# Optimization experiments

Measured on AMD Instinct MI355X. Metric: run time of the kernel, lower is better.

## Reference

```python
import jax, jax.numpy as jnp
import numpy as np

N_NODES = 100000
N_EDGES = 600000
DIM_IN = 128
DIM_H = 128
DIM_OUT = 64
N_LAYERS = 3
BN_EPS = 1e-5


def setup_inputs() -> dict:
    key = jax.random.key(0)
    ks = jax.random.split(key, 10)
    x = jax.random.normal(ks[0], (N_NODES, DIM_IN), dtype=jnp.float32)
    edge_index = jax.random.randint(ks[1], (2, N_EDGES), 0, N_NODES, dtype=jnp.int64)
    s = 0.05
    conv_w1 = jax.random.normal(ks[2], (N_LAYERS, DIM_H, DIM_H), dtype=jnp.float32) * s
    conv_b1 = jnp.zeros((N_LAYERS, DIM_H), jnp.float32)
    conv_w2 = jax.random.normal(ks[3], (N_LAYERS, DIM_H, DIM_H), dtype=jnp.float32) * s
    conv_b2 = jnp.zeros((N_LAYERS, DIM_H), jnp.float32)
    bn_gamma = jnp.ones((N_LAYERS, DIM_H), jnp.float32)
    bn_beta = jnp.zeros((N_LAYERS, DIM_H), jnp.float32)
    fc1_w = jax.random.normal(ks[4], (DIM_H, DIM_H), dtype=jnp.float32) * s
    fc1_b = jnp.zeros((DIM_H,), jnp.float32)
    fc2_w = jax.random.normal(ks[5], (DIM_H, DIM_OUT), dtype=jnp.float32) * s
    fc2_b = jnp.zeros((DIM_OUT,), jnp.float32)
    # deterministic dropout mask, p=0.5, inverted-dropout scaling baked in (0 or 2)
    dropout_mask = (jax.random.uniform(ks[6], (N_NODES, DIM_H)) < 0.5).astype(jnp.float32) * 2.0
    return {"x": x, "edge_index": edge_index,
            "conv_w1": conv_w1, "conv_b1": conv_b1, "conv_w2": conv_w2, "conv_b2": conv_b2,
            "bn_gamma": bn_gamma, "bn_beta": bn_beta,
            "fc1_w": fc1_w, "fc1_b": fc1_b, "fc2_w": fc2_w, "fc2_b": fc2_b,
            "dropout_mask": dropout_mask}


def reference(x, edge_index, conv_w1, conv_b1, conv_w2, conv_b2,
              bn_gamma, bn_beta, fc1_w, fc1_b, fc2_w, fc2_b, dropout_mask):
    src, dst = edge_index[0], edge_index[1]
    n = x.shape[0]
    h = x
    for l in range(N_LAYERS):
        # GINConv (eps=0): (1+eps)*h + sum_{j->i} h_j, then 2-layer MLP
        agg = h + jax.ops.segment_sum(h[src], dst, num_segments=n)
        z = jnp.maximum(agg @ conv_w1[l] + conv_b1[l], 0.0) @ conv_w2[l] + conv_b2[l]
        z = jnp.maximum(z, 0.0)  # outer ReLU
        # BatchNorm1d (training mode: batch stats, biased variance)
        mean = z.mean(axis=0)
        var = z.var(axis=0)
        h = (z - mean) * jax.lax.rsqrt(var + BN_EPS) * bn_gamma[l] + bn_beta[l]
    h = jnp.maximum(h @ fc1_w + fc1_b, 0.0)
    h = h * dropout_mask  # dropout p=0.5 with precomputed inverted mask
    logits = h @ fc2_w + fc2_b
    return jax.nn.log_softmax(logits, axis=-1)
```

## Files before the change

### kernel.cpp

```cpp
#include <hip/hip_runtime.h>
#include <stdint.h>

#define N_NODES 100000
#define N_EDGES 600000
#define DIM_H   128
#define DIM_OUT 64
#define WPAD    136
#define BN_EPS  1e-5f
#define NBLK    391
#define GRID64_HEAD 1563
#define MLP_GRID 782

typedef __attribute__((ext_vector_type(8))) __bf16        bh8;
typedef __attribute__((ext_vector_type(4))) float         fl4;
typedef __attribute__((ext_vector_type(8))) unsigned short us8;
typedef __attribute__((ext_vector_type(4))) unsigned short us4;

__device__ __forceinline__ unsigned short f2bfbits(float f) {
  unsigned int u = __builtin_bit_cast(unsigned int, f);
  u += 0x7fffu + ((u >> 16) & 1u);
  return (unsigned short)(u >> 16);
}
__device__ __forceinline__ float bf2f(unsigned short b) {
  unsigned int u = ((unsigned int)b) << 16;
  return __builtin_bit_cast(float, u);
}
__device__ __forceinline__ void wave_lds_fence() {
  asm volatile("s_waitcnt lgkmcnt(0)" ::: "memory");
  __builtin_amdgcn_sched_barrier(0);
}

__global__ void prep_kernel(const float* __restrict__ cw1, const float* __restrict__ cw2,
                            const float* __restrict__ fc1w, const float* __restrict__ fc2w,
                            unsigned short* __restrict__ W1F, unsigned short* __restrict__ W2F,
                            unsigned short* __restrict__ F1F, unsigned short* __restrict__ F2F,
                            float* __restrict__ stats, int* __restrict__ deg,
                            unsigned short* __restrict__ zrow) {
  int t = blockIdx.x * 256 + threadIdx.x;
  if (t < 3 * 16384) {
    int l = t >> 14, o = t & 16383;
    int j = o & 7, lane = (o >> 3) & 63, kk = (o >> 9) & 3, n0 = o >> 11;
    int k = kk * 32 + ((lane >> 4) << 3) + j;
    int n = (n0 << 4) + (lane & 15);
    W1F[t] = f2bfbits(cw1[l * 16384 + k * 128 + n]);
    W2F[t] = f2bfbits(cw2[l * 16384 + k * 128 + n]);
  }
  if (t < 16384) {
    int o = t;
    int j = o & 7, lane = (o >> 3) & 63, kk = (o >> 9) & 3, n0 = o >> 11;
    int k = kk * 32 + ((lane >> 4) << 3) + j;
    int n = (n0 << 4) + (lane & 15);
    F1F[t] = f2bfbits(fc1w[k * 128 + n]);
  }
  if (t < 8192) {
    int o = t;
    int j = o & 7, lane = (o >> 3) & 63, kk = (o >> 9) & 3, n0 = o >> 11;
    int k = kk * 32 + ((lane >> 4) << 3) + j;
    int n = (n0 << 4) + (lane & 15);
    F2F[t] = f2bfbits(fc2w[k * 64 + n]);
  }
  if (t < 768)   stats[t] = 0.f;
  if (t < 128)   zrow[t] = 0;
  if (t < N_NODES) deg[t] = 0;
}

__global__ void deg_xcast(const float* __restrict__ x, unsigned short* __restrict__ xB,
                          const int* __restrict__ ei, int* __restrict__ deg,
                          const float* __restrict__ mask, unsigned int* __restrict__ bmask) {
  int i = blockIdx.x * 256 + threadIdx.x;
  fl4 v = reinterpret_cast<const fl4*>(x)[i];
  us4 p;
#pragma unroll
  for (int j = 0; j < 4; ++j) p[j] = f2bfbits(v[j]);
  reinterpret_cast<us4*>(xB)[i] = p;
  if (i < N_EDGES) atomicAdd(&deg[ei[N_EDGES + i]], 1);
  if (i < N_NODES * 4) {
    const float* mp = mask + (long)i * 32;
    unsigned int b = 0;
#pragma unroll
    for (int j8 = 0; j8 < 8; ++j8) {
      fl4 mv = *reinterpret_cast<const fl4*>(mp + j8 * 4);
      b |= (mv[0] > 0.f ? 1u : 0u) << (j8 * 4 + 0);
      b |= (mv[1] > 0.f ? 1u : 0u) << (j8 * 4 + 1);
      b |= (mv[2] > 0.f ? 1u : 0u) << (j8 * 4 + 2);
      b |= (mv[3] > 0.f ? 1u : 0u) << (j8 * 4 + 3);
    }
    bmask[i] = b;
  }
}

__global__ void scanA(const int* __restrict__ deg, int* __restrict__ rowstart,
                      int* __restrict__ bsum) {
  __shared__ int s[256];
  int t = threadIdx.x, i = blockIdx.x * 256 + t;
  int v = (i < N_NODES) ? deg[i] : 0;
  s[t] = v;
  __syncthreads();
#pragma unroll
  for (int off = 1; off < 256; off <<= 1) {
    int u = (t >= off) ? s[t - off] : 0;
    __syncthreads();
    s[t] += u;
    __syncthreads();
  }
  if (i < N_NODES) rowstart[i] = s[t] - v;
  if (t == 0) bsum[blockIdx.x] = s[255];
}

__global__ void scanC(int* __restrict__ rowstart, const int* __restrict__ bsum,
                      int* __restrict__ cursor) {
  __shared__ int sred[256];
  int b = blockIdx.x, t = threadIdx.x;
  int partial = 0;
  for (int j = t; j < b; j += 256) partial += bsum[j];
  sred[t] = partial;
  __syncthreads();
#pragma unroll
  for (int off = 128; off > 0; off >>= 1) {
    if (t < off) sred[t] += sred[t + off];
    __syncthreads();
  }
  int boffb = sred[0];
  int i = b * 256 + t;
  if (i < N_NODES) {
    int v = rowstart[i] + boffb;
    rowstart[i] = v;
    cursor[i] = v;
  }
  if (i == 0) rowstart[N_NODES] = N_EDGES;
}

__global__ void csr_fill(const int* __restrict__ ei, int* __restrict__ cursor,
                         int* __restrict__ csr_src) {
  int e = blockIdx.x * 256 + threadIdx.x;
  if (e < N_EDGES) {
    int pos = atomicAdd(&cursor[ei[N_EDGES + e]], 1);
    csr_src[pos] = ei[e];
  }
}

__global__ void bn_finalize(const float* __restrict__ stats, const float* __restrict__ gamma,
                            const float* __restrict__ beta, float* __restrict__ sb) {
  int c = threadIdx.x;
  const float inv_n = 1.0f / (float)N_NODES;
  float mean = stats[c] * inv_n;
  float var  = stats[128 + c] * inv_n - mean * mean;
  float s = gamma[c] * rsqrtf(var + BN_EPS);
  sb[c] = s;
  sb[128 + c] = beta[c] - mean * s;
}

template <int AFFINE>
__global__ __launch_bounds__(256)
void gather_h(const unsigned short* __restrict__ H, const float* __restrict__ sb,
              const int* __restrict__ rowstart, const int* __restrict__ csr,
              unsigned short* __restrict__ aggB) {
  int node = blockIdx.x * 4 + (threadIdx.x >> 6);
  int lane = threadIdx.x & 63;
  int q = lane >> 4, lc = lane & 15;
  int c = lc * 8;

  fl4 scA, scB, bcA, bcB;
  if (AFFINE) {
    scA = *reinterpret_cast<const fl4*>(sb + c);
    scB = *reinterpret_cast<const fl4*>(sb + c + 4);
    bcA = *reinterpret_cast<const fl4*>(sb + 128 + c);
    bcB = *reinterpret_cast<const fl4*>(sb + 128 + c + 4);
  }

  int nodeu = __builtin_amdgcn_readfirstlane(node);
  int rs = rowstart[nodeu], re = rowstart[nodeu + 1];
  int cnt = re - rs + 1;
  float acc[8] = {0.f, 0.f, 0.f, 0.f, 0.f, 0.f, 0.f, 0.f};

  for (int base = 0; base < cnt; base += 64) {
    int item = base + lane;
    int myidx = (item == 0) ? nodeu
              : ((item < cnt) ? csr[rs + item - 1] : N_NODES);
    int lim = cnt - base; if (lim > 64) lim = 64;
    for (int sub = 0; sub < lim; sub += 8) {
      int i0 = __shfl(myidx, sub + q);
      int i1 = __shfl(myidx, sub + 4 + q);
      us8 r0 = *reinterpret_cast<const us8*>(H + (long)i0 * DIM_H + c);
      us8 r1 = *reinterpret_cast<const us8*>(H + (long)i1 * DIM_H + c);
#pragma unroll
      for (int j = 0; j < 8; ++j) acc[j] += bf2f(r0[j]) + bf2f(r1[j]);
    }
  }

#pragma unroll
  for (int j = 0; j < 8; ++j) {
    acc[j] += __shfl_xor(acc[j], 16);
    acc[j] += __shfl_xor(acc[j], 32);
  }

  if (q == 0) {
    us8 pk;
    if (AFFINE) {
      float fc = (float)cnt;
#pragma unroll
      for (int j = 0; j < 4; ++j) {
        pk[j]     = f2bfbits(scA[j] * acc[j]     + fc * bcA[j]);
        pk[4 + j] = f2bfbits(scB[j] * acc[4 + j] + fc * bcB[j]);
      }
    } else {
#pragma unroll
      for (int j = 0; j < 8; ++j) pk[j] = f2bfbits(acc[j]);
    }
    *reinterpret_cast<us8*>(aggB + (long)node * DIM_H + c) = pk;
  }
}

__global__ __launch_bounds__(256, 4)
void mlp_kernel(const unsigned short* __restrict__ A,
                const unsigned short* __restrict__ W1F, const float* __restrict__ b1,
                const unsigned short* __restrict__ W2F, const float* __restrict__ b2,
                unsigned short* __restrict__ Z, float* __restrict__ stats) {
  __shared__ __align__(16) unsigned short ybuf[128 * WPAD];
  __shared__ float red[4][2][128];

  const int tid = threadIdx.x;
  const int wid = tid >> 6, lane = tid & 63;
  const int lr = lane & 15, lg = lane >> 4;
  const int row0 = blockIdx.x * 128;

  bh8 afrag[2][4];
#pragma unroll
  for (int rt = 0; rt < 2; ++rt) {
    int row = row0 + wid * 32 + rt * 16 + lr;
    bool valid = row < N_NODES;
    const unsigned short* ap = A + (long)row * DIM_H;
#pragma unroll
    for (int kk = 0; kk < 4; ++kk) {
      us8 t = (us8)0;
      if (valid) t = *reinterpret_cast<const us8*>(ap + kk * 32 + 8 * lg);
      afrag[rt][kk] = __builtin_bit_cast(bh8, t);
    }
  }

  float bias1[8], bias2[8];
#pragma unroll
  for (int n0 = 0; n0 < 8; ++n0) { bias1[n0] = b1[n0 * 16 + lr]; bias2[n0] = b2[n0 * 16 + lr]; }

  bh8 bnxt[4];
#pragma unroll
  for (int kk = 0; kk < 4; ++kk)
    bnxt[kk] = *reinterpret_cast<const bh8*>(&W1F[(kk << 9) + lane * 8]);

#pragma unroll
  for (int n0 = 0; n0 < 8; ++n0) {
    bh8 bc[4];
#pragma unroll
    for (int kk = 0; kk < 4; ++kk) bc[kk] = bnxt[kk];
    if (n0 < 7) {
#pragma unroll
      for (int kk = 0; kk < 4; ++kk)
        bnxt[kk] = *reinterpret_cast<const bh8*>(&W1F[(((n0 + 1) * 4 + kk) << 9) + lane * 8]);
    }
    fl4 acc[2] = {{0,0,0,0},{0,0,0,0}};
#pragma unroll
    for (int kk = 0; kk < 4; ++kk) {
      acc[0] = __builtin_amdgcn_mfma_f32_16x16x32_bf16(afrag[0][kk], bc[kk], acc[0], 0, 0, 0);
      acc[1] = __builtin_amdgcn_mfma_f32_16x16x32_bf16(afrag[1][kk], bc[kk], acc[1], 0, 0, 0);
    }
#pragma unroll
    for (int rt = 0; rt < 2; ++rt)
#pragma unroll
      for (int r = 0; r < 4; ++r) {
        float v = acc[rt][r] + bias1[n0];
        v = v > 0.f ? v : 0.f;
        ybuf[(wid * 32 + rt * 16 + 4 * lg + r) * WPAD + n0 * 16 + lr] = f2bfbits(v);
      }
  }

#pragma unroll
  for (int kk = 0; kk < 4; ++kk)
    bnxt[kk] = *reinterpret_cast<const bh8*>(&W2F[(kk << 9) + lane * 8]);

  wave_lds_fence();

  bh8 a2[2][4];
#pragma unroll
  for (int rt = 0; rt < 2; ++rt)
#pragma unroll
    for (int kk = 0; kk < 4; ++kk)
      a2[rt][kk] = *reinterpret_cast<const bh8*>(
          &ybuf[(wid * 32 + rt * 16 + lr) * WPAD + kk * 32 + 8 * lg]);

  wave_lds_fence();

#pragma unroll
  for (int n0 = 0; n0 < 8; ++n0) {
    bh8 bc[4];
#pragma unroll
    for (int kk = 0; kk < 4; ++kk) bc[kk] = bnxt[kk];
    if (n0 < 7) {
#pragma unroll
      for (int kk = 0; kk < 4; ++kk)
        bnxt[kk] = *reinterpret_cast<const bh8*>(&W2F[(((n0 + 1) * 4 + kk) << 9) + lane * 8]);
    }
    fl4 acc[2] = {{0,0,0,0},{0,0,0,0}};
#pragma unroll
    for (int kk = 0; kk < 4; ++kk) {
      acc[0] = __builtin_amdgcn_mfma_f32_16x16x32_bf16(a2[0][kk], bc[kk], acc[0], 0, 0, 0);
      acc[1] = __builtin_amdgcn_mfma_f32_16x16x32_bf16(a2[1][kk], bc[kk], acc[1], 0, 0, 0);
    }
    float sp = 0.f, qp = 0.f;
#pragma unroll
    for (int rt = 0; rt < 2; ++rt)
#pragma unroll
      for (int r = 0; r < 4; ++r) {
        int row = row0 + wid * 32 + rt * 16 + 4 * lg + r;
        float v = acc[rt][r] + bias2[n0];
        v = v > 0.f ? v : 0.f;
        ybuf[(wid * 32 + rt * 16 + 4 * lg + r) * WPAD + n0 * 16 + lr] = f2bfbits(v);
        if (row < N_NODES) { sp += v; qp += v * v; }
      }
    sp += __shfl_xor(sp, 16); sp += __shfl_xor(sp, 32);
    qp += __shfl_xor(qp, 16); qp += __shfl_xor(qp, 32);
    if (lg == 0) { red[wid][0][n0 * 16 + lr] = sp; red[wid][1][n0 * 16 + lr] = qp; }
  }

  wave_lds_fence();

#pragma unroll
  for (int i = 0; i < 8; ++i) {
    int ch = i * 64 + lane;
    int r  = wid * 32 + (ch >> 4);
    int c8 = (ch & 15) << 3;
    int row = row0 + r;
    if (row < N_NODES)
      *reinterpret_cast<uint4*>(&Z[(long)row * DIM_H + c8]) =
          *reinterpret_cast<const uint4*>(&ybuf[r * WPAD + c8]);
  }

  __syncthreads();

  {
    int which = tid >> 7, cc = tid & 127;
    float v = red[0][which][cc] + red[1][which][cc] + red[2][which][cc] + red[3][which][cc];
    unsafeAtomicAdd(&stats[which * 128 + cc], v);
  }
}

__global__ __launch_bounds__(256, 6)
void head_kernel(const unsigned short* __restrict__ Z, const float* __restrict__ sb,
                 const unsigned short* __restrict__ F1F, const float* __restrict__ fc1b,
                 const unsigned short* __restrict__ F2F, const float* __restrict__ fc2b,
                 const unsigned int* __restrict__ bmask, float* __restrict__ out) {
  __shared__ __align__(16) unsigned short ybuf[64 * WPAD];

  const int tid = threadIdx.x;
  const int wid = tid >> 6, lane = tid & 63;
  const int lr = lane & 15, lg = lane >> 4;
  const int row0 = blockIdx.x * 64;

  unsigned int bw[4][4];
#pragma unroll
  for (int r = 0; r < 4; ++r) {
    int row = row0 + wid * 16 + 4 * lg + r;
    if (row < N_NODES) {
      uint4 t = *reinterpret_cast<const uint4*>(bmask + (long)row * 4);
      bw[r][0] = t.x; bw[r][1] = t.y; bw[r][2] = t.z; bw[r][3] = t.w;
    } else {
      bw[r][0] = bw[r][1] = bw[r][2] = bw[r][3] = 0u;
    }
  }

  float bias1[8], bias2[4];
#pragma unroll
  for (int n0 = 0; n0 < 8; ++n0) bias1[n0] = fc1b[n0 * 16 + lr];
#pragma unroll
  for (int n0 = 0; n0 < 4; ++n0) bias2[n0] = fc2b[n0 * 16 + lr];

  bh8 afrag[4];
#pragma unroll
  for (int kk = 0; kk < 4; ++kk) {
    int k0 = kk * 32 + 8 * lg;
    fl4 s0  = *reinterpret_cast<const fl4*>(sb + k0);
    fl4 s1  = *reinterpret_cast<const fl4*>(sb + k0 + 4);
    fl4 bb0 = *reinterpret_cast<const fl4*>(sb + 128 + k0);
    fl4 bb1 = *reinterpret_cast<const fl4*>(sb + 128 + k0 + 4);
    int row = row0 + wid * 16 + lr;
    us8 t = (us8)0;
    if (row < N_NODES) {
      us8 zv = *reinterpret_cast<const us8*>(Z + (long)row * DIM_H + k0);
#pragma unroll
      for (int j = 0; j < 4; ++j) {
        t[j]     = f2bfbits(bf2f(zv[j])     * s0[j] + bb0[j]);
        t[4 + j] = f2bfbits(bf2f(zv[4 + j]) * s1[j] + bb1[j]);
      }
    }
    afrag[kk] = __builtin_bit_cast(bh8, t);
  }

  bh8 bnxt[4];
#pragma unroll
  for (int kk = 0; kk < 4; ++kk)
    bnxt[kk] = *reinterpret_cast<const bh8*>(&F1F[(kk << 9) + lane * 8]);
#pragma unroll
  for (int n0 = 0; n0 < 8; ++n0) {
    bh8 bc[4];
#pragma unroll
    for (int kk = 0; kk < 4; ++kk) bc[kk] = bnxt[kk];
    if (n0 < 7) {
#pragma unroll
      for (int kk = 0; kk < 4; ++kk)
        bnxt[kk] = *reinterpret_cast<const bh8*>(&F1F[(((n0 + 1) * 4 + kk) << 9) + lane * 8]);
    }
    fl4 acc = {0.f, 0.f, 0.f, 0.f};
#pragma unroll
    for (int kk = 0; kk < 4; ++kk)
      acc = __builtin_amdgcn_mfma_f32_16x16x32_bf16(afrag[kk], bc[kk], acc, 0, 0, 0);
#pragma unroll
    for (int r = 0; r < 4; ++r) {
      float v = acc[r] + bias1[n0];
      v = v > 0.f ? v : 0.f;
      float mk = ((bw[r][n0 >> 1] >> (((n0 & 1) << 4) + lr)) & 1u) ? 2.0f : 0.0f;
      ybuf[(wid * 16 + 4 * lg + r) * WPAD + n0 * 16 + lr] = f2bfbits(v * mk);
    }
  }

#pragma unroll
  for (int kk = 0; kk < 4; ++kk)
    bnxt[kk] = *reinterpret_cast<const bh8*>(&F2F[(kk << 9) + lane * 8]);

  wave_lds_fence();

  bh8 a2[4];
#pragma unroll
  for (int kk = 0; kk < 4; ++kk)
    a2[kk] = *reinterpret_cast<const bh8*>(
        &ybuf[(wid * 16 + lr) * WPAD + kk * 32 + 8 * lg]);

  fl4 acc2[4];
#pragma unroll
  for (int n0 = 0; n0 < 4; ++n0) {
    bh8 bc[4];
#pragma unroll
    for (int kk = 0; kk < 4; ++kk) bc[kk] = bnxt[kk];
    if (n0 < 3) {
#pragma unroll
      for (int kk = 0; kk < 4; ++kk)
        bnxt[kk] = *reinterpret_cast<const bh8*>(&F2F[(((n0 + 1) * 4 + kk) << 9) + lane * 8]);
    }
    acc2[n0] = (fl4){0.f, 0.f, 0.f, 0.f};
#pragma unroll
    for (int kk = 0; kk < 4; ++kk)
      acc2[n0] = __builtin_amdgcn_mfma_f32_16x16x32_bf16(a2[kk], bc[kk], acc2[n0], 0, 0, 0);
#pragma unroll
    for (int r = 0; r < 4; ++r) acc2[n0][r] += bias2[n0];
  }

#pragma unroll
  for (int r = 0; r < 4; ++r) {
    float m = fmaxf(fmaxf(acc2[0][r], acc2[1][r]), fmaxf(acc2[2][r], acc2[3][r]));
#pragma unroll
    for (int d = 1; d < 16; d <<= 1) m = fmaxf(m, __shfl_xor(m, d, 16));
    float se = 0.f;
#pragma unroll
    for (int n0 = 0; n0 < 4; ++n0) se += __expf(acc2[n0][r] - m);
#pragma unroll
    for (int d = 1; d < 16; d <<= 1) se += __shfl_xor(se, d, 16);
    float lse = m + __logf(se);
    int row = row0 + wid * 16 + 4 * lg + r;
    if (row < N_NODES) {
#pragma unroll
      for (int n0 = 0; n0 < 4; ++n0)
        out[(long)row * DIM_OUT + n0 * 16 + lr] = acc2[n0][r] - lse;
    }
  }
}

extern "C" void kernel_launch(void* const* d_in, const int* in_sizes, int n_in,
                              void* d_out, int out_size, void* d_ws, size_t ws_size,
                              hipStream_t stream) {
  const float* x      = (const float*)d_in[0];
  const int*   ei     = (const int*)d_in[1];
  const float* cw1    = (const float*)d_in[2];
  const float* cb1    = (const float*)d_in[3];
  const float* cw2    = (const float*)d_in[4];
  const float* cb2    = (const float*)d_in[5];
  const float* gamma  = (const float*)d_in[6];
  const float* beta   = (const float*)d_in[7];
  const float* fc1w   = (const float*)d_in[8];
  const float* fc1b   = (const float*)d_in[9];
  const float* fc2w   = (const float*)d_in[10];
  const float* fc2b   = (const float*)d_in[11];
  const float* mask   = (const float*)d_in[12];
  float* out = (float*)d_out;

  char* ws = (char*)d_ws;
  unsigned short* aggB  = (unsigned short*)ws;
  unsigned short* Zb    = (unsigned short*)(ws + 25600000);
  unsigned short* W1F   = (unsigned short*)(ws + 51200256);
  unsigned short* W2F   = (unsigned short*)(ws + 51298560);
  unsigned short* F1F   = (unsigned short*)(ws + 51396864);
  unsigned short* F2F   = (unsigned short*)(ws + 51429632);
  float*          stats = (float*)(ws + 51446016);
  int*            rowst = (int*)(ws + 51449088);
  int*            cursor= (int*)(ws + 51849092);
  int*            csr   = (int*)(ws + 52249092);
  int*            bsum  = (int*)(ws + 54649092);
  unsigned int*   bmask = (unsigned int*)(ws + 54650656);
  float*          sb    = (float*)(ws + 56250656);
  if (ws_size < 56253728u) return;

  prep_kernel<<<NBLK, 256, 0, stream>>>(cw1, cw2, fc1w, fc2w, W1F, W2F, F1F, F2F,
                                        stats, cursor, Zb + (long)N_NODES * DIM_H);
  deg_xcast<<<12500, 256, 0, stream>>>(x, Zb, ei, cursor, mask, bmask);

  scanA<<<NBLK, 256, 0, stream>>>(cursor, rowst, bsum);
  scanC<<<NBLK, 256, 0, stream>>>(rowst, bsum, cursor);
  csr_fill<<<2344, 256, 0, stream>>>(ei, cursor, csr);

  gather_h<0><<<25000, 256, 0, stream>>>(Zb, nullptr, rowst, csr, aggB);
  mlp_kernel<<<MLP_GRID, 256, 0, stream>>>(aggB, W1F, cb1, W2F, cb2, Zb, stats);
  bn_finalize<<<1, 128, 0, stream>>>(stats, gamma, beta, sb);

  gather_h<1><<<25000, 256, 0, stream>>>(Zb, sb, rowst, csr, aggB);
  mlp_kernel<<<MLP_GRID, 256, 0, stream>>>(aggB, W1F + 16384, cb1 + 128, W2F + 16384,
                                           cb2 + 128, Zb, stats + 256);
  bn_finalize<<<1, 128, 0, stream>>>(stats + 256, gamma + 128, beta + 128, sb + 256);

  gather_h<1><<<25000, 256, 0, stream>>>(Zb, sb + 256, rowst, csr, aggB);
  mlp_kernel<<<MLP_GRID, 256, 0, stream>>>(aggB, W1F + 32768, cb1 + 256, W2F + 32768,
                                           cb2 + 256, Zb, stats + 512);
  bn_finalize<<<1, 128, 0, stream>>>(stats + 512, gamma + 256, beta + 256, sb + 512);

  head_kernel<<<GRID64_HEAD, 256, 0, stream>>>(Zb, sb + 512,
                                               F1F, fc1b, F2F, fc2b, bmask, out);
}
```

Measured before the change: 309.6 us.

## Gather two nodes per wave and shrink MLP tile to 64 rows

The gather kernel now assigns two destination nodes to each wave, issuing four row loads per step instead of two for more memory-level parallelism, and launches half the blocks. The MLP kernel's row tile drops from 128 to 64 rows per block, with a smaller LDS buffer and occupancy hint raised from 4 to 6, to increase occupancy and block count. The costs are wasted work when the paired nodes' degrees differ (looping to the max count) and more per-block weight reloads in the MLP.

After: 355.9 us. 15.0% more time.

```diff
diff --git a/kernel.cpp b/kernel.cpp
--- a/kernel.cpp
+++ b/kernel.cpp
@@ -8,8 +8,7 @@
 #define WPAD    136
 #define BN_EPS  1e-5f
 #define NBLK    391
-#define GRID64_HEAD 1563
-#define MLP_GRID 782
+#define GRID64  1563
 
 typedef __attribute__((ext_vector_type(8))) __bf16        bh8;
 typedef __attribute__((ext_vector_type(4))) float         fl4;
@@ -155,7 +154,7 @@
 void gather_h(const unsigned short* __restrict__ H, const float* __restrict__ sb,
               const int* __restrict__ rowstart, const int* __restrict__ csr,
               unsigned short* __restrict__ aggB) {
-  int node = blockIdx.x * 4 + (threadIdx.x >> 6);
+  int pair = blockIdx.x * 4 + (threadIdx.x >> 6);
   int lane = threadIdx.x & 63;
   int q = lane >> 4, lc = lane & 15;
   int c = lc * 8;
@@ -168,73 +167,91 @@
     bcB = *reinterpret_cast<const fl4*>(sb + 128 + c + 4);
   }
 
-  int nodeu = __builtin_amdgcn_readfirstlane(node);
-  int rs = rowstart[nodeu], re = rowstart[nodeu + 1];
-  int cnt = re - rs + 1;
-  float acc[8] = {0.f, 0.f, 0.f, 0.f, 0.f, 0.f, 0.f, 0.f};
-
-  for (int base = 0; base < cnt; base += 64) {
+  int pairu = __builtin_amdgcn_readfirstlane(pair);
+  int node0 = pairu * 2, node1 = node0 + 1;
+  int rs0 = rowstart[node0], re0 = rowstart[node0 + 1], re1 = rowstart[node1 + 1];
+  int rs1 = re0;
+  int cnt0 = re0 - rs0 + 1, cnt1 = re1 - rs1 + 1;
+  int cmax = cnt0 > cnt1 ? cnt0 : cnt1;
+
+  float acc0[8] = {0,0,0,0,0,0,0,0}, acc1[8] = {0,0,0,0,0,0,0,0};
+
+  for (int base = 0; base < cmax; base += 64) {
     int item = base + lane;
-    int myidx = (item == 0) ? nodeu
-              : ((item < cnt) ? csr[rs + item - 1] : N_NODES);
-    int lim = cnt - base; if (lim > 64) lim = 64;
+    int c0 = rs0 + item - 1; c0 = c0 < 0 ? 0 : (c0 >= N_EDGES ? N_EDGES - 1 : c0);
+    int c1 = rs1 + item - 1; c1 = c1 < 0 ? 0 : (c1 >= N_EDGES ? N_EDGES - 1 : c1);
+    int v0 = csr[c0], v1 = csr[c1];
+    int myidx0 = (item == 0) ? node0 : ((item < cnt0) ? v0 : N_NODES);
+    int myidx1 = (item == 0) ? node1 : ((item < cnt1) ? v1 : N_NODES);
+    int lim = cmax - base; if (lim > 64) lim = 64;
     for (int sub = 0; sub < lim; sub += 8) {
-      int i0 = __shfl(myidx, sub + q);
-      int i1 = __shfl(myidx, sub + 4 + q);
-      us8 r0 = *reinterpret_cast<const us8*>(H + (long)i0 * DIM_H + c);
-      us8 r1 = *reinterpret_cast<const us8*>(H + (long)i1 * DIM_H + c);
-#pragma unroll
-      for (int j = 0; j < 8; ++j) acc[j] += bf2f(r0[j]) + bf2f(r1[j]);
+      int i00 = __shfl(myidx0, sub + q);
+      int i01 = __shfl(myidx0, sub + 4 + q);
+      int i10 = __shfl(myidx1, sub + q);
+      int i11 = __shfl(myidx1, sub + 4 + q);
+      us8 r00 = *reinterpret_cast<const us8*>(H + (long)i00 * DIM_H + c);
+      us8 r01 = *reinterpret_cast<const us8*>(H + (long)i01 * DIM_H + c);
+      us8 r10 = *reinterpret_cast<const us8*>(H + (long)i10 * DIM_H + c);
+      us8 r11 = *reinterpret_cast<const us8*>(H + (long)i11 * DIM_H + c);
+#pragma unroll
+      for (int j = 0; j < 8; ++j) {
+        acc0[j] += bf2f(r00[j]) + bf2f(r01[j]);
+        acc1[j] += bf2f(r10[j]) + bf2f(r11[j]);
+      }
     }
   }
 
 #pragma unroll
   for (int j = 0; j < 8; ++j) {
-    acc[j] += __shfl_xor(acc[j], 16);
-    acc[j] += __shfl_xor(acc[j], 32);
-  }
-
-  if (q == 0) {
+    acc0[j] += __shfl_xor(acc0[j], 16);
+    acc0[j] += __shfl_xor(acc0[j], 32);
+    acc1[j] += __shfl_xor(acc1[j], 16);
+    acc1[j] += __shfl_xor(acc1[j], 32);
+  }
+
+  if (q < 2) {
+    int node = q == 0 ? node0 : node1;
+    float cntf = (float)(q == 0 ? cnt0 : cnt1);
     us8 pk;
     if (AFFINE) {
-      float fc = (float)cnt;
 #pragma unroll
       for (int j = 0; j < 4; ++j) {
-        pk[j]     = f2bfbits(scA[j] * acc[j]     + fc * bcA[j]);
-        pk[4 + j] = f2bfbits(scB[j] * acc[4 + j] + fc * bcB[j]);
+        float a = q == 0 ? acc0[j] : acc1[j];
+        float b = q == 0 ? acc0[4 + j] : acc1[4 + j];
+        pk[j]     = f2bfbits(scA[j] * a + cntf * bcA[j]);
+        pk[4 + j] = f2bfbits(scB[j] * b + cntf * bcB[j]);
       }
     } else {
 #pragma unroll
-      for (int j = 0; j < 8; ++j) pk[j] = f2bfbits(acc[j]);
+      for (int j = 0; j < 8; ++j) pk[j] = f2bfbits(q == 0 ? acc0[j] : acc1[j]);
     }
     *reinterpret_cast<us8*>(aggB + (long)node * DIM_H + c) = pk;
   }
 }
 
-__global__ __launch_bounds__(256, 4)
+__global__ __launch_bounds__(256, 6)
 void mlp_kernel(const unsigned short* __restrict__ A,
                 const unsigned short* __restrict__ W1F, const float* __restrict__ b1,
                 const unsigned short* __restrict__ W2F, const float* __restrict__ b2,
                 unsigned short* __restrict__ Z, float* __restrict__ stats) {
-  __shared__ __align__(16) unsigned short ybuf[128 * WPAD];
+  __shared__ __align__(16) unsigned short ybuf[64 * WPAD];
   __shared__ float red[4][2][128];
 
   const int tid = threadIdx.x;
   const int wid = tid >> 6, lane = tid & 63;
   const int lr = lane & 15, lg = lane >> 4;
-  const int row0 = blockIdx.x * 128;
-
-  bh8 afrag[2][4];
-#pragma unroll
-  for (int rt = 0; rt < 2; ++rt) {
-    int row = row0 + wid * 32 + rt * 16 + lr;
+  const int row0 = blockIdx.x * 64;
+
+  bh8 afrag[4];
+  {
+    int row = row0 + wid * 16 + lr;
     bool valid = row < N_NODES;
     const unsigned short* ap = A + (long)row * DIM_H;
 #pragma unroll
     for (int kk = 0; kk < 4; ++kk) {
       us8 t = (us8)0;
       if (valid) t = *reinterpret_cast<const us8*>(ap + kk * 32 + 8 * lg);
-      afrag[rt][kk] = __builtin_bit_cast(bh8, t);
+      afrag[kk] = __builtin_bit_cast(bh8, t);
     }
   }
 
@@ -257,20 +274,16 @@
       for (int kk = 0; kk < 4; ++kk)
         bnxt[kk] = *reinterpret_cast<const bh8*>(&W1F[(((n0 + 1) * 4 + kk) << 9) + lane * 8]);
     }
-    fl4 acc[2] = {{0,0,0,0},{0,0,0,0}};
-#pragma unroll
-    for (int kk = 0; kk < 4; ++kk) {
-      acc[0] = __builtin_amdgcn_mfma_f32_16x16x32_bf16(afrag[0][kk], bc[kk], acc[0], 0, 0, 0);
-      acc[1] = __builtin_amdgcn_mfma_f32_16x16x32_bf16(afrag[1][kk], bc[kk], acc[1], 0, 0, 0);
-    }
-#pragma unroll
-    for (int rt = 0; rt < 2; ++rt)
-#pragma unroll
-      for (int r = 0; r < 4; ++r) {
-        float v = acc[rt][r] + bias1[n0];
-        v = v > 0.f ? v : 0.f;
-        ybuf[(wid * 32 + rt * 16 + 4 * lg + r) * WPAD + n0 * 16 + lr] = f2bfbits(v);
-      }
+    fl4 acc = {0.f, 0.f, 0.f, 0.f};
+#pragma unroll
+    for (int kk = 0; kk < 4; ++kk)
+      acc = __builtin_amdgcn_mfma_f32_16x16x32_bf16(afrag[kk], bc[kk], acc, 0, 0, 0);
+#pragma unroll
+    for (int r = 0; r < 4; ++r) {
+      float v = acc[r] + bias1[n0];
+      v = v > 0.f ? v : 0.f;
+      ybuf[(wid * 16 + 4 * lg + r) * WPAD + n0 * 16 + lr] = f2bfbits(v);
+    }
   }
 
 #pragma unroll
@@ -279,13 +292,11 @@
 
   wave_lds_fence();
 
-  bh8 a2[2][4];
-#pragma unroll
-  for (int rt = 0; rt < 2; ++rt)
-#pragma unroll
-    for (int kk = 0; kk < 4; ++kk)
-      a2[rt][kk] = *reinterpret_cast<const bh8*>(
-          &ybuf[(wid * 32 + rt * 16 + lr) * WPAD + kk * 32 + 8 * lg]);
+  bh8 a2[4];
+#pragma unroll
+  for (int kk = 0; kk < 4; ++kk)
+    a2[kk] = *reinterpret_cast<const bh8*>(
+        &ybuf[(wid * 16 + lr) * WPAD + kk * 32 + 8 * lg]);
 
   wave_lds_fence();
 
@@ -299,23 +310,19 @@
       for (int kk = 0; kk < 4; ++kk)
         bnxt[kk] = *reinterpret_cast<const bh8*>(&W2F[(((n0 + 1) * 4 + kk) << 9) + lane * 8]);
     }
-    fl4 acc[2] = {{0,0,0,0},{0,0,0,0}};
-#pragma unroll
-    for (int kk = 0; kk < 4; ++kk) {
-      acc[0] = __builtin_amdgcn_mfma_f32_16x16x32_bf16(a2[0][kk], bc[kk], acc[0], 0, 0, 0);
-      acc[1] = __builtin_amdgcn_mfma_f32_16x16x32_bf16(a2[1][kk], bc[kk], acc[1], 0, 0, 0);
-    }
+    fl4 acc = {0.f, 0.f, 0.f, 0.f};
+#pragma unroll
+    for (int kk = 0; kk < 4; ++kk)
+      acc = __builtin_amdgcn_mfma_f32_16x16x32_bf16(a2[kk], bc[kk], acc, 0, 0, 0);
     float sp = 0.f, qp = 0.f;
 #pragma unroll
-    for (int rt = 0; rt < 2; ++rt)
-#pragma unroll
-      for (int r = 0; r < 4; ++r) {
-        int row = row0 + wid * 32 + rt * 16 + 4 * lg + r;
-        float v = acc[rt][r] + bias2[n0];
-        v = v > 0.f ? v : 0.f;
-        ybuf[(wid * 32 + rt * 16 + 4 * lg + r) * WPAD + n0 * 16 + lr] = f2bfbits(v);
-        if (row < N_NODES) { sp += v; qp += v * v; }
-      }
+    for (int r = 0; r < 4; ++r) {
+      int row = row0 + wid * 16 + 4 * lg + r;
+      float v = acc[r] + bias2[n0];
+      v = v > 0.f ? v : 0.f;
+      ybuf[(wid * 16 + 4 * lg + r) * WPAD + n0 * 16 + lr] = f2bfbits(v);
+      if (row < N_NODES) { sp += v; qp += v * v; }
+    }
     sp += __shfl_xor(sp, 16); sp += __shfl_xor(sp, 32);
     qp += __shfl_xor(qp, 16); qp += __shfl_xor(qp, 32);
     if (lg == 0) { red[wid][0][n0 * 16 + lr] = sp; red[wid][1][n0 * 16 + lr] = qp; }
@@ -324,9 +331,9 @@
   wave_lds_fence();
 
 #pragma unroll
-  for (int i = 0; i < 8; ++i) {
+  for (int i = 0; i < 4; ++i) {
     int ch = i * 64 + lane;
-    int r  = wid * 32 + (ch >> 4);
+    int r  = wid * 16 + (ch >> 4);
     int c8 = (ch & 15) << 3;
     int row = row0 + r;
     if (row < N_NODES)
@@ -514,20 +521,20 @@
   scanC<<<NBLK, 256, 0, stream>>>(rowst, bsum, cursor);
   csr_fill<<<2344, 256, 0, stream>>>(ei, cursor, csr);
 
-  gather_h<0><<<25000, 256, 0, stream>>>(Zb, nullptr, rowst, csr, aggB);
-  mlp_kernel<<<MLP_GRID, 256, 0, stream>>>(aggB, W1F, cb1, W2F, cb2, Zb, stats);
+  gather_h<0><<<12500, 256, 0, stream>>>(Zb, nullptr, rowst, csr, aggB);
+  mlp_kernel<<<GRID64, 256, 0, stream>>>(aggB, W1F, cb1, W2F, cb2, Zb, stats);
   bn_finalize<<<1, 128, 0, stream>>>(stats, gamma, beta, sb);
 
-  gather_h<1><<<25000, 256, 0, stream>>>(Zb, sb, rowst, csr, aggB);
-  mlp_kernel<<<MLP_GRID, 256, 0, stream>>>(aggB, W1F + 16384, cb1 + 128, W2F + 16384,
-                                           cb2 + 128, Zb, stats + 256);
+  gather_h<1><<<12500, 256, 0, stream>>>(Zb, sb, rowst, csr, aggB);
+  mlp_kernel<<<GRID64, 256, 0, stream>>>(aggB, W1F + 16384, cb1 + 128, W2F + 16384,
+                                         cb2 + 128, Zb, stats + 256);
   bn_finalize<<<1, 128, 0, stream>>>(stats + 256, gamma + 128, beta + 128, sb + 256);
 
-  gather_h<1><<<25000, 256, 0, stream>>>(Zb, sb + 256, rowst, csr, aggB);
-  mlp_kernel<<<MLP_GRID, 256, 0, stream>>>(aggB, W1F + 32768, cb1 + 256, W2F + 32768,
-                                           cb2 + 256, Zb, stats + 512);
+  gather_h<1><<<12500, 256, 0, stream>>>(Zb, sb + 256, rowst, csr, aggB);
+  mlp_kernel<<<GRID64, 256, 0, stream>>>(aggB, W1F + 32768, cb1 + 256, W2F + 32768,
+                                         cb2 + 256, Zb, stats + 512);
   bn_finalize<<<1, 128, 0, stream>>>(stats + 512, gamma + 256, beta + 256, sb + 512);
 
-  head_kernel<<<GRID64_HEAD, 256, 0, stream>>>(Zb, sb + 512,
-                                               F1F, fc1b, F2F, fc2b, bmask, out);
-}
+  head_kernel<<<GRID64, 256, 0, stream>>>(Zb, sb + 512,
+                                          F1F, fc1b, F2F, fc2b, bmask, out);
+}
```
